# Kernel optimization log

Hardware: AMD Instinct MI355X
Metric: run time of the kernel (lower is better)

The kernel has to match this reference:

```python
import jax, jax.numpy as jnp
import numpy as np

EPS = 1e-6
SLIDING_WINDOW = 512
ROPE_BASE = 10000.0  # rope_local_base_freq for sliding_attention layers


def _rms_norm(x, w=None):
    # Gemma-style RMSNorm computed in fp32 then cast back
    xf = x.astype(jnp.float32)
    out = xf * jax.lax.rsqrt(jnp.mean(xf * xf, axis=-1, keepdims=True) + EPS)
    if w is not None:
        out = out * w.astype(jnp.float32)
    return out.astype(x.dtype)


def _rotate_half(x):
    x1, x2 = jnp.split(x, 2, axis=-1)
    return jnp.concatenate((-x2, x1), axis=-1)


def setup_inputs() -> dict:
    key = jax.random.key(0)
    ks = jax.random.split(key, 6)
    B, S, H, NH, NKV, D = 1, 4096, 2048, 8, 2, 256
    hidden_states = jax.random.normal(ks[0], (B, S, H), dtype=jnp.float32)
    w_q = jax.random.normal(ks[1], (H, NH * D), dtype=jnp.float32) * 0.02
    w_k = jax.random.normal(ks[2], (H, NKV * D), dtype=jnp.float32) * 0.02
    w_v = jax.random.normal(ks[3], (H, NKV * D), dtype=jnp.float32) * 0.02
    w_o = jax.random.normal(ks[4], (NH * D, H), dtype=jnp.float32) * 0.02
    q_norm_w = jnp.ones((D,), dtype=jnp.float32)
    k_norm_w = jnp.ones((D,), dtype=jnp.float32)
    # RoPE tables (local base freq, sliding layer)
    inv_freq = 1.0 / (ROPE_BASE ** (jnp.arange(0, D, 2, dtype=jnp.float32) / D))
    pos = jnp.arange(S, dtype=jnp.float32)
    freqs = pos[:, None] * inv_freq[None, :]          # [S, D/2]
    emb = jnp.concatenate((freqs, freqs), axis=-1)    # [S, D]
    cos = jnp.broadcast_to(jnp.cos(emb)[None], (B, S, D)).astype(jnp.float32)
    sin = jnp.broadcast_to(jnp.sin(emb)[None], (B, S, D)).astype(jnp.float32)
    return {"hidden_states": hidden_states, "w_q": w_q, "w_k": w_k, "w_v": w_v,
            "w_o": w_o, "q_norm_w": q_norm_w, "k_norm_w": k_norm_w,
            "cos": cos, "sin": sin}


def reference(hidden_states, w_q, w_k, w_v, w_o, q_norm_w, k_norm_w, cos, sin):
    B, S, _ = hidden_states.shape
    D = cos.shape[-1]
    NH = w_q.shape[1] // D
    NKV = w_k.shape[1] // D
    G = NH // NKV

    # projections -> [B, S, heads, D], per-head RMSNorm (Gemma3n-style)
    q = _rms_norm((hidden_states @ w_q).reshape(B, S, NH, D), q_norm_w)
    k = _rms_norm((hidden_states @ w_k).reshape(B, S, NKV, D), k_norm_w)
    v = _rms_norm((hidden_states @ w_v).reshape(B, S, NKV, D))  # v_norm: no scale

    q = q.transpose(0, 2, 1, 3)  # [B, NH, S, D]
    k = k.transpose(0, 2, 1, 3)  # [B, NKV, S, D]
    v = v.transpose(0, 2, 1, 3)

    # RoPE, cos/sin unsqueezed over the head dim
    c = cos[:, None, :, :]
    s = sin[:, None, :, :]
    q = q * c + _rotate_half(q) * s
    k = k * c + _rotate_half(k) * s

    # GQA: repeat KV heads
    k = jnp.repeat(k, G, axis=1)  # [B, NH, S, D]
    v = jnp.repeat(v, G, axis=1)

    # attention, scaling = 1.0 (q_norm replaces 1/sqrt(d) in this family)
    scores = jnp.einsum('bhqd,bhkd->bhqk', q, k)

    # causal + sliding-window mask
    i = jnp.arange(S)[:, None]
    j = jnp.arange(S)[None, :]
    mask = (j <= i) & ((i - j) < SLIDING_WINDOW)
    scores = jnp.where(mask[None, None], scores, jnp.finfo(scores.dtype).min)

    attn = jax.nn.softmax(scores.astype(jnp.float32), axis=-1).astype(q.dtype)
    out = jnp.einsum('bhqk,bhkd->bhqd', attn, v)
    out = out.transpose(0, 2, 1, 3).reshape(B, S, NH * D)
    return out @ w_o
```

## Files before the change

### kernel.cpp

```cpp
#include <hip/hip_runtime.h>
#include <hip/hip_bf16.h>

#define S_LEN 4096
#define HDIM  2048
#define NHQ   8
#define NKVH  2
#define DHEAD 256
#define WIN   512
#define NQKV  3072

typedef __hip_bfloat16 bf16_t;
using fragAB = __attribute__((ext_vector_type(8))) short;
using fragC  = __attribute__((ext_vector_type(4))) float;

struct __align__(8)  bf16x4 { bf16_t v[4]; };
struct __align__(16) bf16x8 { bf16_t v[8]; };

typedef unsigned int u32;
typedef const __attribute__((address_space(1))) u32* gas_ptr;
typedef __attribute__((address_space(3))) u32* las_ptr;

__device__ __forceinline__ void async_copy16(const void* g, void* l) {
  __builtin_amdgcn_global_load_lds((gas_ptr)g, (las_ptr)l, 16, 0, 0);
}

#define NEG_BIG (-3.0e38f)

__device__ __forceinline__ void split2(float x, bf16_t& hi, bf16_t& lo) {
  bf16_t h = __float2bfloat16(x);
  hi = h;
  lo = __float2bfloat16(x - (float)h);
}

__global__ __launch_bounds__(256) void prep0(
    const float* __restrict__ hid, bf16_t* __restrict__ hidh,
    bf16_t* __restrict__ hidl, const float* __restrict__ wq,
    const float* __restrict__ wk, const float* __restrict__ wv,
    bf16_t* __restrict__ hiT, bf16_t* __restrict__ loT) {
  __shared__ bf16_t th[32][33];
  __shared__ bf16_t tl[32][33];
  int bx = blockIdx.x;
  if (bx < 4096) {
    int i = (bx * 256 + threadIdx.x) * 8;
    float4 a = *(const float4*)(hid + i);
    float4 b = *(const float4*)(hid + i + 4);
    float xs[8] = {a.x, a.y, a.z, a.w, b.x, b.y, b.z, b.w};
    bf16x8 hv, lv;
#pragma unroll
    for (int j = 0; j < 8; ++j) split2(xs[j], hv.v[j], lv.v[j]);
    *(bf16x8*)(hidh + i) = hv;
    *(bf16x8*)(hidl + i) = lv;
  } else {
    int b2 = bx - 4096;
    int oc = (b2 % 96) * 32;
    int r0 = (b2 / 96) * 32;
    const float* src; int C, c0;
    if (oc < 2048)      { src = wq; C = 2048; c0 = oc; }
    else if (oc < 2560) { src = wk; C = 512;  c0 = oc - 2048; }
    else                { src = wv; C = 512;  c0 = oc - 2560; }
    int tx = threadIdx.x & 31, ty = threadIdx.x >> 5;
#pragma unroll
    for (int i = 0; i < 4; ++i) {
      float x = src[(size_t)(r0 + ty + i * 8) * C + c0 + tx];
      bf16_t h, l; split2(x, h, l);
      th[ty + i * 8][tx] = h;
      tl[ty + i * 8][tx] = l;
    }
    __syncthreads();
#pragma unroll
    for (int i = 0; i < 4; ++i) {
      hiT[(size_t)(oc + ty + i * 8) * HDIM + r0 + tx] = th[tx][ty + i * 8];
      loT[(size_t)(oc + ty + i * 8) * HDIM + r0 + tx] = tl[tx][ty + i * 8];
    }
  }
}

#define VMCNT_(n) asm volatile("s_waitcnt vmcnt(" #n ")" ::: "memory")
#define VMCNT(n) VMCNT_(n)
#define BARRIER()                     \
  {                                   \
    asm volatile("" ::: "memory");    \
    __builtin_amdgcn_s_barrier();     \
    asm volatile("" ::: "memory");    \
  }

#define MFMA_(a, b, c) __builtin_amdgcn_mfma_f32_16x16x32_bf16(a, b, c, 0, 0, 0)

#define OFF_AH 0
#define OFF_AL 16384
#define OFF_BH 32768
#define OFF_BL 45056
#define BUFSZ  57344

#define SPLIT_STEP()                                                    \
  {                                                                     \
    fragAB bh[3], bl[3];                                                \
    _Pragma("unroll") for (int j = 0; j < 3; ++j) {                     \
      const char* bp = bufc + (wn + j * 16 + l16) * 64 + rdq;           \
      bh[j] = *(const fragAB*)(bp + OFF_BH);                            \
      bl[j] = *(const fragAB*)(bp + OFF_BL);                            \
    }                                                                   \
    _Pragma("unroll") for (int p = 0; p < 2; ++p) {                     \
      fragAB ah[2], al[2];                                              \
      _Pragma("unroll") for (int u = 0; u < 2; ++u) {                   \
        const char* ap = bufc + (wm + (2 * p + u) * 16 + l16) * 64 + rdq;\
        ah[u] = *(const fragAB*)(ap + OFF_AH);                          \
        al[u] = *(const fragAB*)(ap + OFF_AL);                          \
      }                                                                 \
      __builtin_amdgcn_s_setprio(1);                                    \
      _Pragma("unroll") for (int j = 0; j < 3; ++j)                     \
        _Pragma("unroll") for (int u = 0; u < 2; ++u)                   \
          acc[2 * p + u][j] = MFMA_(al[u], bh[j], acc[2 * p + u][j]);   \
      _Pragma("unroll") for (int j = 0; j < 3; ++j)                     \
        _Pragma("unroll") for (int u = 0; u < 2; ++u)                   \
          acc[2 * p + u][j] = MFMA_(ah[u], bl[j], acc[2 * p + u][j]);   \
      _Pragma("unroll") for (int j = 0; j < 3; ++j)                     \
        _Pragma("unroll") for (int u = 0; u < 2; ++u)                   \
          acc[2 * p + u][j] = MFMA_(ah[u], bh[j], acc[2 * p + u][j]);   \
      __builtin_amdgcn_s_setprio(0);                                    \
    }                                                                   \
  }

__global__ __launch_bounds__(1024, 4) void gemm_split2(
    const bf16_t* __restrict__ Ah, const bf16_t* __restrict__ Al,
    const bf16_t* __restrict__ Bh, const bf16_t* __restrict__ Bl,
    float* __restrict__ C, int M, int N, int K) {
  __shared__ __align__(16) char lds[2 * BUFSZ];
  const int t = threadIdx.x;
  const int wave = t >> 6, lane = t & 63;
  const int quad = lane >> 4, l16 = lane & 15;
  const int g = blockIdx.y * 16 + blockIdx.x;
  const int lby = (g & 7) * 2 + ((g >> 3) >> 4);
  const int lbx = (g >> 3) & 15;
  const int m0 = lby * 256, n0 = lbx * 192;
  const int wm = (wave >> 2) * 64, wn = (wave & 3) * 48;
  const int rdq = (quad ^ ((l16 >> 1) & 3)) * 16;

  const size_t laneOff =
      (size_t)(lane >> 2) * K * 2 + 16 * ((lane & 3) ^ ((lane >> 3) & 3));

  const char* gbase[4];
  int ldsOff[4];
  const int nch = (wave < 8) ? 4 : 3;
#pragma unroll
  for (int pos = 0; pos < 4; ++pos) {
    int c = (pos < 3) ? (wave + 16 * pos) : (48 + wave);
    const char* gb; int lo;
    if (c < 12)      { gb = (const char*)Bh + (size_t)(n0 + 16 * c) * K * 2;        lo = OFF_BH + c * 1024; }
    else if (c < 24) { gb = (const char*)Bl + (size_t)(n0 + 16 * (c - 12)) * K * 2; lo = OFF_BL + (c - 12) * 1024; }
    else if (c < 40) { gb = (const char*)Ah + (size_t)(m0 + 16 * (c - 24)) * K * 2; lo = OFF_AH + (c - 24) * 1024; }
    else             { gb = (const char*)Al + (size_t)(m0 + 16 * (c - 40)) * K * 2; lo = OFF_AL + (c - 40) * 1024; }
    gbase[pos] = gb;
    ldsOff[pos] = lo;
  }

  fragC zero4 = {0.f, 0.f, 0.f, 0.f};
  fragC acc[4][3];
#pragma unroll
  for (int i = 0; i < 4; ++i)
#pragma unroll
    for (int j = 0; j < 3; ++j) acc[i][j] = zero4;

  char* ldsc = (char*)lds;
  for (int ps = 0; ps < nch; ++ps)
    async_copy16(gbase[ps] + laneOff, ldsc + ldsOff[ps]);

  size_t kk = 64;
  int cur = 0;
  const int NS = K / 32;
  for (int it = 0; it < NS - 1; ++it) {
    const char* bufc = ldsc + cur * BUFSZ;
    char* nb = ldsc + (cur ^ 1) * BUFSZ;
    VMCNT(0); BARRIER();
    for (int ps = 0; ps < nch; ++ps)
      async_copy16(gbase[ps] + kk + laneOff, nb + ldsOff[ps]);
    kk += 64;
    SPLIT_STEP();
    cur ^= 1;
  }
  {
    const char* bufc = ldsc + cur * BUFSZ;
    VMCNT(0); BARRIER();
    SPLIT_STEP();
  }

#pragma unroll
  for (int i = 0; i < 4; ++i)
#pragma unroll
    for (int j = 0; j < 3; ++j)
#pragma unroll
      for (int r = 0; r < 4; ++r) {
        int row = m0 + wm + i * 16 + quad * 4 + r;
        int col = n0 + wn + j * 16 + l16;
        C[(size_t)row * N + col] = acc[i][j][r];
      }
}

#define BT_OFF_A 0
#define BT_OFF_B 32768
#define BT_BUFSZ 49152

#define BT_STEP()                                                         \
  {                                                                       \
    fragAB bfr[2][2];                                                     \
    _Pragma("unroll") for (int j = 0; j < 2; ++j)                         \
      _Pragma("unroll") for (int ks = 0; ks < 2; ++ks)                    \
        bfr[j][ks] = *(const fragAB*)(bufc + BT_OFF_B +                   \
                                      (wn + j * 16 + l16) * 128 +         \
                                      (((ks * 4 + quad) ^ rx) * 16));     \
    _Pragma("unroll") for (int p = 0; p < 2; ++p) {                       \
      fragAB af[2][2];                                                    \
      _Pragma("unroll") for (int u = 0; u < 2; ++u)                       \
        _Pragma("unroll") for (int ks = 0; ks < 2; ++ks)                  \
          af[u][ks] = *(const fragAB*)(bufc + BT_OFF_A +                  \
                                       (wm + (2 * p + u) * 16 + l16) * 128 + \
                                       (((ks * 4 + quad) ^ rx) * 16));    \
      __builtin_amdgcn_s_setprio(1);                                      \
      _Pragma("unroll") for (int ks = 0; ks < 2; ++ks)                    \
        _Pragma("unroll") for (int j = 0; j < 2; ++j)                     \
          _Pragma("unroll") for (int u = 0; u < 2; ++u)                   \
            acc[2 * p + u][j] = MFMA_(af[u][ks], bfr[j][ks], acc[2 * p + u][j]); \
      __builtin_amdgcn_s_setprio(0);                                      \
    }                                                                     \
  }

__global__ __launch_bounds__(1024, 4) void gemm_bt2(
    const bf16_t* __restrict__ A, const bf16_t* __restrict__ Bt,
    float* __restrict__ C, int M, int N, int K) {
  __shared__ __align__(16) char lds[2 * BT_BUFSZ];
  const int t = threadIdx.x;
  const int wave = t >> 6, lane = t & 63;
  const int quad = lane >> 4, l16 = lane & 15;
  const int g = blockIdx.y * 16 + blockIdx.x;
  const int lby = (g & 7) * 2 + ((g >> 3) >> 4);
  const int lbx = (g >> 3) & 15;
  const int m0 = lby * 256, n0 = lbx * 128;
  const int wm = (wave >> 2) * 64, wn = (wave & 3) * 32;
  const int rx = l16 & 7;

  const size_t laneOff =
      (size_t)(lane >> 3) * K * 2 + 16 * ((lane & 7) ^ ((lane >> 3) & 7));

  const char* gbase[3];
  int ldsOff[3];
#pragma unroll
  for (int pos = 0; pos < 3; ++pos) {
    int c = wave + 16 * pos;
    if (c < 16) {
      gbase[pos]  = (const char*)Bt + (size_t)(n0 + 8 * c) * K * 2;
      ldsOff[pos] = BT_OFF_B + c * 1024;
    } else {
      gbase[pos]  = (const char*)A + (size_t)(m0 + 8 * (c - 16)) * K * 2;
      ldsOff[pos] = BT_OFF_A + (c - 16) * 1024;
    }
  }

  fragC zero4 = {0.f, 0.f, 0.f, 0.f};
  fragC acc[4][2];
#pragma unroll
  for (int i = 0; i < 4; ++i)
#pragma unroll
    for (int j = 0; j < 2; ++j) acc[i][j] = zero4;

  char* ldsc = (char*)lds;
#pragma unroll
  for (int ps = 0; ps < 3; ++ps)
    async_copy16(gbase[ps] + laneOff, ldsc + ldsOff[ps]);

  size_t kk = 128;
  int cur = 0;
  const int NS = K / 64;
  for (int it = 0; it < NS - 1; ++it) {
    const char* bufc = ldsc + cur * BT_BUFSZ;
    char* nb = ldsc + (cur ^ 1) * BT_BUFSZ;
    VMCNT(0); BARRIER();
#pragma unroll
    for (int ps = 0; ps < 3; ++ps)
      async_copy16(gbase[ps] + kk + laneOff, nb + ldsOff[ps]);
    kk += 128;
    BT_STEP();
    cur ^= 1;
  }
  {
    const char* bufc = ldsc + cur * BT_BUFSZ;
    VMCNT(0); BARRIER();
    BT_STEP();
  }

#pragma unroll
  for (int i = 0; i < 4; ++i)
#pragma unroll
    for (int j = 0; j < 2; ++j)
#pragma unroll
      for (int r = 0; r < 4; ++r) {
        int row = m0 + wm + i * 16 + quad * 4 + r;
        int col = n0 + wn + j * 16 + l16;
        C[(size_t)row * N + col] = acc[i][j][r];
      }
}

__global__ __launch_bounds__(256) void prep2(
    const float* __restrict__ proj, const float* __restrict__ qnw,
    const float* __restrict__ knw, const float* __restrict__ cosb,
    const float* __restrict__ sinb, bf16_t* __restrict__ qhi,
    bf16_t* __restrict__ qlo, bf16_t* __restrict__ khi,
    bf16_t* __restrict__ klo, bf16_t* __restrict__ vt,
    const float* __restrict__ wo, bf16_t* __restrict__ woT) {
  __shared__ float rs_[32];
  __shared__ bf16_t tile[32][33];
  int bx = blockIdx.x;
  if (bx < 10240) {
    const int wv = threadIdx.x >> 6, lane = threadIdx.x & 63;
    const int idx = bx * 4 + wv;
    const int s = idx / (NHQ + NKVH), hb = idx % (NHQ + NKVH);
    const float* w; bf16_t* oh; bf16_t* ol; int inOff, outStride, oBase;
    if (hb < NHQ) {
      w = qnw; oh = qhi; ol = qlo;
      inOff = hb * DHEAD; outStride = NHQ * DHEAD; oBase = hb * DHEAD;
    } else {
      int hk = hb - NHQ;
      w = knw; oh = khi; ol = klo;
      inOff = NHQ * DHEAD + hk * DHEAD; outStride = NKVH * DHEAD; oBase = hk * DHEAD;
    }
    const int d = lane * 4;
    float4 x = *(const float4*)(proj + (size_t)s * NQKV + inOff + d);
    float ss = x.x * x.x + x.y * x.y + x.z * x.z + x.w * x.w;
    ss += __shfl_xor(ss, 1);  ss += __shfl_xor(ss, 2);  ss += __shfl_xor(ss, 4);
    ss += __shfl_xor(ss, 8);  ss += __shfl_xor(ss, 16); ss += __shfl_xor(ss, 32);
    float r = rsqrtf(ss * (1.0f / DHEAD) + 1e-6f);
    float4 w4 = *(const float4*)(w + d);
    float xn[4] = {x.x * r * w4.x, x.y * r * w4.y, x.z * r * w4.z, x.w * r * w4.w};
    float ot[4];
#pragma unroll
    for (int j = 0; j < 4; ++j) ot[j] = __shfl_xor(xn[j], 32);
    float sgn = (lane < 32) ? -1.0f : 1.0f;
    float4 c4 = *(const float4*)(cosb + (size_t)s * DHEAD + d);
    float4 s4 = *(const float4*)(sinb + (size_t)s * DHEAD + d);
    float cc[4] = {c4.x, c4.y, c4.z, c4.w};
    float sn[4] = {s4.x, s4.y, s4.z, s4.w};
    bf16x4 hv, lv;
#pragma unroll
    for (int j = 0; j < 4; ++j) {
      float y = xn[j] * cc[j] + sgn * ot[j] * sn[j];
      split2(y, hv.v[j], lv.v[j]);
    }
    size_t o = (size_t)s * outStride + oBase + d;
    *(bf16x4*)(oh + o) = hv;
    *(bf16x4*)(ol + o) = lv;
  } else if (bx < 10240 + 256) {
    int b2 = bx - 10240;
    int s0 = (b2 & 127) * 32, hh = b2 >> 7;
    const int inOff = NHQ * DHEAD + NKVH * DHEAD;
    const float* base = proj + (size_t)s0 * NQKV + inOff + hh * DHEAD;
    int t = threadIdx.x;
    int sl = t >> 3, c8 = t & 7;
    const float4* rowp = (const float4*)(base + (size_t)sl * NQKV + c8 * 32);
    float ss = 0.f;
#pragma unroll
    for (int i = 0; i < 8; ++i) {
      float4 v = rowp[i];
      ss += v.x * v.x + v.y * v.y + v.z * v.z + v.w * v.w;
    }
    ss += __shfl_xor(ss, 1); ss += __shfl_xor(ss, 2); ss += __shfl_xor(ss, 4);
    if (c8 == 0) rs_[sl] = rsqrtf(ss * (1.0f / DHEAD) + 1e-6f);
    __syncthreads();
    int tx = t & 31, ty = t >> 5;
#pragma unroll
    for (int ch = 0; ch < 8; ++ch) {
#pragma unroll
      for (int i = 0; i < 4; ++i) {
        int s_ = ty + i * 8;
        float x = base[(size_t)s_ * NQKV + ch * 32 + tx];
        tile[s_][tx] = __float2bfloat16(x * rs_[s_]);
      }
      __syncthreads();
#pragma unroll
      for (int i = 0; i < 4; ++i) {
        int dl = ty + i * 8;
        vt[((size_t)hh * DHEAD + ch * 32 + dl) * S_LEN + s0 + tx] = tile[tx][dl];
      }
      __syncthreads();
    }
  } else {
    int b2 = bx - 10496;
    int c0 = (b2 & 63) * 32, r0 = (b2 >> 6) * 32;
    int tx = threadIdx.x & 31, ty = threadIdx.x >> 5;
#pragma unroll
    for (int i = 0; i < 4; ++i)
      tile[ty + i * 8][tx] =
          __float2bfloat16(wo[(size_t)(r0 + ty + i * 8) * HDIM + c0 + tx]);
    __syncthreads();
#pragma unroll
    for (int i = 0; i < 4; ++i)
      woT[(size_t)(c0 + ty + i * 8) * (NHQ * DHEAD) + r0 + tx] = tile[tx][ty + i * 8];
  }
}

__global__ __launch_bounds__(512, 2) void attn_split(
    const bf16_t* __restrict__ Qhi, const bf16_t* __restrict__ Qlo,
    const bf16_t* __restrict__ Khi, const bf16_t* __restrict__ Klo,
    const bf16_t* __restrict__ Vt, bf16_t* __restrict__ Aout) {
  const int g = blockIdx.y * 32 + blockIdx.x;
  const int lbx = (g & 7) * 4 + ((g >> 3) & 3);
  const int h = g >> 5;
  const int qb = lbx * 128;
  const int wave = threadIdx.x >> 6, lane = threadIdx.x & 63;
  const int quad = lane >> 4, l16 = lane & 15;
  const int qw = qb + wave * 16;
  const int kv = h >> 2;
  const bf16_t* Qh_ = Qhi + h * DHEAD;
  const bf16_t* Ql_ = Qlo + h * DHEAD;
  const bf16_t* Kh_ = Khi + kv * DHEAD;
  const bf16_t* Kl_ = Klo + kv * DHEAD;
  const bf16_t* Vh_ = Vt + (size_t)kv * DHEAD * S_LEN;

  __shared__ __align__(16) bf16_t KshH[2][32 * 256];
  __shared__ __align__(16) bf16_t KshL[2][32 * 256];
  __shared__ __align__(16) bf16_t Vsh[2][256 * 32];
  __shared__ __align__(16) bf16_t Plds[8][16 * 32];

  fragAB qfh[8], qfl[8];
#pragma unroll
  for (int c = 0; c < 8; ++c) {
    size_t off = (size_t)(qw + l16) * (NHQ * DHEAD) + c * 32 + quad * 8;
    qfh[c] = *(const fragAB*)(Qh_ + off);
    qfl[c] = *(const fragAB*)(Ql_ + off);
  }

  int kRow[2], kCol[2], vRow[2], vCol[2];
#pragma unroll
  for (int i = 0; i < 2; ++i) {
    int ci = i * 512 + threadIdx.x;
    kRow[i] = ci >> 5;
    kCol[i] = ((ci & 31) ^ (kRow[i] & 31)) * 8;
    vRow[i] = ci >> 2;
    vCol[i] = ((ci & 3) ^ (vRow[i] & 3)) * 8;
  }

#define ASTAGE(buf, kb_)                                                     \
  _Pragma("unroll")                                                          \
  for (int i = 0; i < 2; ++i) {                                              \
    size_t dst = (size_t)(i * 512 + threadIdx.x) * 16;                       \
    size_t koff = (size_t)((kb_) + kRow[i]) * (NKVH * DHEAD) + kCol[i];      \
    async_copy16(Kh_ + koff, (char*)KshH[buf] + dst);                        \
    async_copy16(Kl_ + koff, (char*)KshL[buf] + dst);                        \
    async_copy16(Vh_ + (size_t)vRow[i] * S_LEN + (kb_) + vCol[i],            \
                 (char*)Vsh[buf] + dst);                                     \
  }

  fragC zero4 = {0.f, 0.f, 0.f, 0.f};
  fragC o_acc[16];
#pragma unroll
  for (int c = 0; c < 16; ++c) o_acc[c] = zero4;
  float m_run[4] = {NEG_BIG, NEG_BIG, NEG_BIG, NEG_BIG};
  float l_run[4] = {0.f, 0.f, 0.f, 0.f};
  const float LOG2E = 1.4426950408889634f;

  int k_lo = qb - (WIN - 1);
  if (k_lo < 0) k_lo = 0;
  k_lo &= ~31;

  ASTAGE(0, k_lo);
  int cur = 0;

  for (int kb = k_lo; kb < qb + 128; kb += 32) {
    VMCNT(0); BARRIER();
    if (kb + 32 < qb + 128) {
      int nbuf = cur ^ 1;
      ASTAGE(nbuf, kb + 32);
    }
    const char* KH = (const char*)KshH[cur];
    const char* KL = (const char*)KshL[cur];
    const char* VB = (const char*)Vsh[cur];

    fragC s[2] = {zero4, zero4};
    __builtin_amdgcn_s_setprio(1);
#pragma unroll
    for (int c = 0; c < 8; ++c) {
      int j = c * 4 + quad;
#pragma unroll
      for (int gg = 0; gg < 2; ++gg) {
        int row = gg * 16 + l16;
        int off = (row * 32 + (j ^ (row & 31))) * 16;
        fragAB kh = *(const fragAB*)(KH + off);
        fragAB kl = *(const fragAB*)(KL + off);
        s[gg] = __builtin_amdgcn_mfma_f32_16x16x32_bf16(qfl[c], kh, s[gg], 0, 0, 0);
        s[gg] = __builtin_amdgcn_mfma_f32_16x16x32_bf16(qfh[c], kl, s[gg], 0, 0, 0);
        s[gg] = __builtin_amdgcn_mfma_f32_16x16x32_bf16(qfh[c], kh, s[gg], 0, 0, 0);
      }
    }
    __builtin_amdgcn_s_setprio(0);

    float p[2][4], alpha[4];
#pragma unroll
    for (int r = 0; r < 4; ++r) {
      int qi = qw + quad * 4 + r;
      bool vld[2];
      float mx = NEG_BIG;
#pragma unroll
      for (int gg = 0; gg < 2; ++gg) {
        int ki = kb + gg * 16 + l16;
        vld[gg] = (ki <= qi) && (qi - ki < WIN);
        mx = fmaxf(mx, vld[gg] ? s[gg][r] : NEG_BIG);
      }
      mx = fmaxf(mx, __shfl_xor(mx, 1));
      mx = fmaxf(mx, __shfl_xor(mx, 2));
      mx = fmaxf(mx, __shfl_xor(mx, 4));
      mx = fmaxf(mx, __shfl_xor(mx, 8));
      float mn = fmaxf(m_run[r], mx);
      float a  = exp2f(fmaxf(m_run[r] - mn, -80.f) * LOG2E);
      float rs = 0.f;
#pragma unroll
      for (int gg = 0; gg < 2; ++gg) {
        float e = vld[gg] ? exp2f(fmaxf(s[gg][r] - mn, -80.f) * LOG2E) : 0.f;
        p[gg][r] = e;
        rs += e;
      }
      rs += __shfl_xor(rs, 1);
      rs += __shfl_xor(rs, 2);
      rs += __shfl_xor(rs, 4);
      rs += __shfl_xor(rs, 8);
      l_run[r] = l_run[r] * a + rs;
      m_run[r] = mn;
      alpha[r] = a;
    }
#pragma unroll
    for (int c = 0; c < 16; ++c)
#pragma unroll
      for (int r = 0; r < 4; ++r) o_acc[c][r] *= alpha[r];

    bf16_t* Pw = Plds[wave];
#pragma unroll
    for (int r = 0; r < 4; ++r)
#pragma unroll
      for (int gg = 0; gg < 2; ++gg)
        Pw[(quad * 4 + r) * 32 + gg * 16 + l16] = __float2bfloat16(p[gg][r]);
    fragAB pf = *(const fragAB*)((const char*)Pw + l16 * 64 + quad * 16);

    __builtin_amdgcn_s_setprio(1);
#pragma unroll
    for (int c = 0; c < 16; ++c) {
      int d = c * 16 + l16;
      int offv = (d * 4 + (quad ^ (d & 3))) * 16;
      fragAB vf = *(const fragAB*)(VB + offv);
      o_acc[c] = __builtin_amdgcn_mfma_f32_16x16x32_bf16(pf, vf, o_acc[c], 0, 0, 0);
    }
    __builtin_amdgcn_s_setprio(0);
    cur ^= 1;
  }

  float inv_l[4];
#pragma unroll
  for (int r = 0; r < 4; ++r) inv_l[r] = 1.0f / l_run[r];
#pragma unroll
  for (int c = 0; c < 16; ++c)
#pragma unroll
    for (int r = 0; r < 4; ++r) {
      int row = qw + quad * 4 + r;
      int col = h * DHEAD + c * 16 + l16;
      Aout[(size_t)row * (NHQ * DHEAD) + col] = __float2bfloat16(o_acc[c][r] * inv_l[r]);
    }
#undef ASTAGE
}

extern "C" void kernel_launch(void* const* d_in, const int* in_sizes, int n_in,
                              void* d_out, int out_size, void* d_ws, size_t ws_size,
                              hipStream_t stream) {
  const float* hid  = (const float*)d_in[0];
  const float* w_q  = (const float*)d_in[1];
  const float* w_k  = (const float*)d_in[2];
  const float* w_v  = (const float*)d_in[3];
  const float* w_o  = (const float*)d_in[4];
  const float* qnw  = (const float*)d_in[5];
  const float* knw  = (const float*)d_in[6];
  const float* cosb = (const float*)d_in[7];
  const float* sinb = (const float*)d_in[8];
  float* outp = (float*)d_out;

  const size_t M1 = 1048576;
  bf16_t* w = (bf16_t*)d_ws;
  bf16_t* hidh  = w;
  bf16_t* qh    = w;
  bf16_t* hidl  = w + 8 * M1;
  bf16_t* ql    = w + 8 * M1;
  bf16_t* wTh   = w + 16 * M1;
  bf16_t* kh    = w + 16 * M1;
  bf16_t* kl    = w + 18 * M1;
  bf16_t* vt    = w + 20 * M1;
  bf16_t* wTl   = w + 22 * M1;
  bf16_t* woT   = w + 22 * M1;
  float*  projqkv = (float*)(w + 28 * M1);
  bf16_t* aout  = w + 28 * M1;

  prep0<<<4096 + 96 * 64, 256, 0, stream>>>(
      hid, hidh, hidl, w_q, w_k, w_v, wTh, wTl);

  gemm_split2<<<dim3(NQKV / 192, S_LEN / 256), 1024, 0, stream>>>(
      hidh, hidl, wTh, wTl, projqkv, S_LEN, NQKV, HDIM);

  prep2<<<10240 + 256 + 4096, 256, 0, stream>>>(
      projqkv, qnw, knw, cosb, sinb, qh, ql, kh, kl, vt, w_o, woT);

  attn_split<<<dim3(S_LEN / 128, NHQ), 512, 0, stream>>>(qh, ql, kh, kl, vt, aout);

  gemm_bt2<<<dim3(HDIM / 128, S_LEN / 256), 1024, 0, stream>>>(
      aout, woT, outp, S_LEN, HDIM, NHQ * DHEAD);
}
```

Measured before the change: 396.0 us.

## Use 12 waves with 64x64 warp tiles in split-bf16 QKV GEMM

The QKV projection GEMM drops from 16 waves (64x48 per wave) to 12 waves (64x64 per wave), so each wave reuses every loaded A/B fragment over more MFMAs. Global-to-LDS async loads are reassigned so only the first 8 waves issue them, 7 chunks each. This cuts LDS read traffic per MFMA, in exchange for more accumulator registers per wave, fewer waves to hide latency, and less even load issue across waves.

```diff
diff --git a/kernel.cpp b/kernel.cpp
--- a/kernel.cpp
+++ b/kernel.cpp
@@ -94,8 +94,8 @@
 
 #define SPLIT_STEP()                                                    \
   {                                                                     \
-    fragAB bh[3], bl[3];                                                \
-    _Pragma("unroll") for (int j = 0; j < 3; ++j) {                     \
+    fragAB bh[4], bl[4];                                                \
+    _Pragma("unroll") for (int j = 0; j < 4; ++j) {                     \
       const char* bp = bufc + (wn + j * 16 + l16) * 64 + rdq;           \
       bh[j] = *(const fragAB*)(bp + OFF_BH);                            \
       bl[j] = *(const fragAB*)(bp + OFF_BL);                            \
@@ -108,20 +108,20 @@
         al[u] = *(const fragAB*)(ap + OFF_AL);                          \
       }                                                                 \
       __builtin_amdgcn_s_setprio(1);                                    \
-      _Pragma("unroll") for (int j = 0; j < 3; ++j)                     \
+      _Pragma("unroll") for (int j = 0; j < 4; ++j)                     \
         _Pragma("unroll") for (int u = 0; u < 2; ++u)                   \
           acc[2 * p + u][j] = MFMA_(al[u], bh[j], acc[2 * p + u][j]);   \
-      _Pragma("unroll") for (int j = 0; j < 3; ++j)                     \
+      _Pragma("unroll") for (int j = 0; j < 4; ++j)                     \
         _Pragma("unroll") for (int u = 0; u < 2; ++u)                   \
           acc[2 * p + u][j] = MFMA_(ah[u], bl[j], acc[2 * p + u][j]);   \
-      _Pragma("unroll") for (int j = 0; j < 3; ++j)                     \
+      _Pragma("unroll") for (int j = 0; j < 4; ++j)                     \
         _Pragma("unroll") for (int u = 0; u < 2; ++u)                   \
           acc[2 * p + u][j] = MFMA_(ah[u], bh[j], acc[2 * p + u][j]);   \
       __builtin_amdgcn_s_setprio(0);                                    \
     }                                                                   \
   }
 
-__global__ __launch_bounds__(1024, 4) void gemm_split2(
+__global__ __launch_bounds__(768, 3) void gemm_split2(
     const bf16_t* __restrict__ Ah, const bf16_t* __restrict__ Al,
     const bf16_t* __restrict__ Bh, const bf16_t* __restrict__ Bl,
     float* __restrict__ C, int M, int N, int K) {
@@ -133,37 +133,49 @@
   const int lby = (g & 7) * 2 + ((g >> 3) >> 4);
   const int lbx = (g >> 3) & 15;
   const int m0 = lby * 256, n0 = lbx * 192;
-  const int wm = (wave >> 2) * 64, wn = (wave & 3) * 48;
+  const int wm = (wave / 3) * 64, wn = (wave % 3) * 64;
   const int rdq = (quad ^ ((l16 >> 1) & 3)) * 16;
 
   const size_t laneOff =
       (size_t)(lane >> 2) * K * 2 + 16 * ((lane & 3) ^ ((lane >> 3) & 3));
 
-  const char* gbase[4];
-  int ldsOff[4];
-  const int nch = (wave < 8) ? 4 : 3;
-#pragma unroll
-  for (int pos = 0; pos < 4; ++pos) {
-    int c = (pos < 3) ? (wave + 16 * pos) : (48 + wave);
-    const char* gb; int lo;
-    if (c < 12)      { gb = (const char*)Bh + (size_t)(n0 + 16 * c) * K * 2;        lo = OFF_BH + c * 1024; }
-    else if (c < 24) { gb = (const char*)Bl + (size_t)(n0 + 16 * (c - 12)) * K * 2; lo = OFF_BL + (c - 12) * 1024; }
-    else if (c < 40) { gb = (const char*)Ah + (size_t)(m0 + 16 * (c - 24)) * K * 2; lo = OFF_AH + (c - 24) * 1024; }
-    else             { gb = (const char*)Al + (size_t)(m0 + 16 * (c - 40)) * K * 2; lo = OFF_AL + (c - 40) * 1024; }
-    gbase[pos] = gb;
-    ldsOff[pos] = lo;
+  const char* gbase[7];
+  int ldsOff[7];
+  if (wave < 8) {
+#pragma unroll
+    for (int pos = 0; pos < 3; ++pos) {
+      int c = wave + 8 * pos;
+      if (c < 12) {
+        gbase[pos]  = (const char*)Bh + (size_t)(n0 + 16 * c) * K * 2;
+        ldsOff[pos] = OFF_BH + c * 1024;
+      } else {
+        gbase[pos]  = (const char*)Bl + (size_t)(n0 + 16 * (c - 12)) * K * 2;
+        ldsOff[pos] = OFF_BL + (c - 12) * 1024;
+      }
+    }
+#pragma unroll
+    for (int p = 0; p < 4; ++p) {
+      int sub = wave & 3;
+      int R0 = ((sub >> 1) & 1) * 128 + 32 * p + (sub & 1) * 16;
+      const char* base = (const char*)(wave < 4 ? Ah : Al);
+      gbase[3 + p]  = base + (size_t)(m0 + R0) * K * 2;
+      ldsOff[3 + p] = (wave < 4 ? OFF_AH : OFF_AL) + R0 * 64;
+    }
   }
 
   fragC zero4 = {0.f, 0.f, 0.f, 0.f};
-  fragC acc[4][3];
+  fragC acc[4][4];
 #pragma unroll
   for (int i = 0; i < 4; ++i)
 #pragma unroll
-    for (int j = 0; j < 3; ++j) acc[i][j] = zero4;
+    for (int j = 0; j < 4; ++j) acc[i][j] = zero4;
 
   char* ldsc = (char*)lds;
-  for (int ps = 0; ps < nch; ++ps)
-    async_copy16(gbase[ps] + laneOff, ldsc + ldsOff[ps]);
+  if (wave < 8) {
+#pragma unroll
+    for (int ps = 0; ps < 7; ++ps)
+      async_copy16(gbase[ps] + laneOff, ldsc + ldsOff[ps]);
+  }
 
   size_t kk = 64;
   int cur = 0;
@@ -172,8 +184,11 @@
     const char* bufc = ldsc + cur * BUFSZ;
     char* nb = ldsc + (cur ^ 1) * BUFSZ;
     VMCNT(0); BARRIER();
-    for (int ps = 0; ps < nch; ++ps)
-      async_copy16(gbase[ps] + kk + laneOff, nb + ldsOff[ps]);
+    if (wave < 8) {
+#pragma unroll
+      for (int ps = 0; ps < 7; ++ps)
+        async_copy16(gbase[ps] + kk + laneOff, nb + ldsOff[ps]);
+    }
     kk += 64;
     SPLIT_STEP();
     cur ^= 1;
@@ -187,7 +202,7 @@
 #pragma unroll
   for (int i = 0; i < 4; ++i)
 #pragma unroll
-    for (int j = 0; j < 3; ++j)
+    for (int j = 0; j < 4; ++j)
 #pragma unroll
       for (int r = 0; r < 4; ++r) {
         int row = m0 + wm + i * 16 + quad * 4 + r;
@@ -595,7 +610,7 @@
   prep0<<<4096 + 96 * 64, 256, 0, stream>>>(
       hid, hidh, hidl, w_q, w_k, w_v, wTh, wTl);
 
-  gemm_split2<<<dim3(NQKV / 192, S_LEN / 256), 1024, 0, stream>>>(
+  gemm_split2<<<dim3(NQKV / 192, S_LEN / 256), 768, 0, stream>>>(
       hidh, hidl, wTh, wTl, projqkv, S_LEN, NQKV, HDIM);
 
   prep2<<<10240 + 256 + 4096, 256, 0, stream>>>(
```

Measured after the change: 390.5 us. About the same (-1.4%).
